# Kernel optimization log

Hardware: AMD Instinct MI355X
Metric: run time of the kernel (lower is better)

The kernel has to match this reference:

```python
import jax, jax.numpy as jnp
import numpy as np

K_HOP = 2

def _graph_conv(x, A, W, b):
    feats = [x]
    xk = x
    for _ in range(K_HOP):
        xk = jnp.einsum('bmn,bnc->bmc', A, xk)
        feats.append(xk)
    return jnp.concatenate(feats, -1) @ W + b

def _pair_mlp(y, W2, b2, W1, b1, shape):
    # normal_conv: fc1(relu(fc2(y))).reshape(shape)
    return (jax.nn.relu(y @ W2 + b2) @ W1 + b1).reshape(shape)

def setup_inputs():
    key = jax.random.key(0)
    ks = jax.random.split(key, 16)
    B, T, N = 8, 12, 200
    C_IN, H, D, H_ST = 2, 64, 32, 64
    def lin(k, fi, fo):
        k1, k2 = jax.random.split(k)
        s = 1.0 / float(np.sqrt(fi))
        return (jax.random.uniform(k1, (fi, fo), jnp.float32, -s, s),
                jax.random.uniform(k2, (fo,), jnp.float32, -s, s))
    W_s2d, b_s2d = lin(ks[0], H_ST, D)
    W_rz, b_rz = lin(ks[1], 1 + D, 2 * D)
    W_h, b_h = lin(ks[2], 1 + D, D)
    Wc2, bc2 = lin(ks[3], 2 * D, D)
    Wc1, bc1 = lin(ks[4], D, 1)
    Wm2, bm2 = lin(ks[5], 2 * D, D)
    Wm1, bm1 = lin(ks[6], D, 1)
    gin = (C_IN + H) * (1 + K_HOP)
    W_ru, b_ru = lin(ks[7], gin, 2 * H)
    W_cand, b_cand = lin(ks[8], gin, H)
    Wp1, bp1 = lin(ks[9], H, H)
    Wp2, bp2 = lin(ks[10], H, 1)
    x = jax.random.normal(ks[11], (B, T, N, C_IN), jnp.float32)
    node_fea_st = jax.random.normal(ks[12], (N, H_ST), jnp.float32)
    return dict(x=x, node_fea_st=node_fea_st, W_s2d=W_s2d, b_s2d=b_s2d,
                W_rz=W_rz, b_rz=b_rz, W_h=W_h, b_h=b_h,
                Wc2=Wc2, bc2=bc2, Wc1=Wc1, bc1=bc1,
                Wm2=Wm2, bm2=bm2, Wm1=Wm1, bm1=bm1,
                W_ru=W_ru, b_ru=b_ru, W_cand=W_cand, b_cand=b_cand,
                Wp1=Wp1, bp1=bp1, Wp2=Wp2, bp2=bp2)

def reference(x, node_fea_st, W_s2d, b_s2d, W_rz, b_rz, W_h, b_h,
              Wc2, bc2, Wc1, bc1, Wm2, bm2, Wm1, bm1,
              W_ru, b_ru, W_cand, b_cand, Wp1, bp1, Wp2, bp2):
    B, T, N, _ = x.shape
    H = W_cand.shape[1]
    D = W_h.shape[1]
    # states_dy init: linear_s2d(node_fea_st) broadcast over batch
    state_dy0 = jnp.broadcast_to((node_fea_st @ W_s2d + b_s2d)[None], (B, N, D))
    state0 = jnp.zeros((B, N, H), x.dtype)
    xs = jnp.transpose(x, (1, 0, 2, 3))  # [T,B,N,C]

    def step(carry, xt):
        state, state_dy = carry
        inp1 = xt[..., :1]
        # DynamicGraphGRU (conv_method='normal')
        rz = jax.nn.sigmoid(jnp.concatenate([inp1, state_dy], -1) @ W_rz + b_rz)
        r, z = jnp.split(rz, 2, -1)
        h = jnp.tanh(jnp.concatenate([inp1, r * state_dy], -1) @ W_h + b_h)
        new_dy = z * state_dy + (1.0 - z) * h
        s = jax.nn.relu(new_dy)  # [B,N,D]
        y = jnp.concatenate([jnp.broadcast_to(s[:, :, None, :], (B, N, N, D)),
                             jnp.broadcast_to(s[:, None, :, :], (B, N, N, D))], -1)
        g = _pair_mlp(y, Wc2, bc2, Wc1, bc1, (B, N, N))
        m = _pair_mlp(y, Wm2, bm2, Wm1, bm1, (B, N, N))
        A = g * jax.nn.sigmoid(m)  # dynamic graph [B,N,N]
        # DCGRUCell with supports=[A]
        ru = jax.nn.sigmoid(_graph_conv(jnp.concatenate([xt, state], -1), A, W_ru, b_ru))
        rr, u = jnp.split(ru, 2, -1)
        c = jnp.tanh(_graph_conv(jnp.concatenate([xt, rr * state], -1), A, W_cand, b_cand))
        new_state = u * state + (1.0 - u) * c
        return (new_state, new_dy), A

    (state, _), dy_graphs = jax.lax.scan(step, (state0, state_dy0), xs)
    # predictor: Linear -> LeakyReLU -> Linear
    pred = jax.nn.leaky_relu(state @ Wp1 + bp1) @ Wp2 + bp2  # [B,N,1]
    return pred, dy_graphs
```

## Files before the change

kernel.cpp:

```cpp
#include <hip/hip_runtime.h>
#include <math.h>

#define B_ 8
#define T_ 12
#define N_ 200
#define R_ 1600
#define NN_ 40000

__device__ __forceinline__ float sigm(float v) { return 1.f / (1.f + expf(-v)); }

__global__ void __launch_bounds__(256) k_dyall(
        const float* __restrict__ x,  const float* __restrict__ nf,
        const float* __restrict__ Ws2d, const float* __restrict__ bs2d,
        const float* __restrict__ Wrz,  const float* __restrict__ brz,
        const float* __restrict__ Wh,   const float* __restrict__ bh,
        const float* __restrict__ Wc2,  const float* __restrict__ Wm2,
        const float* __restrict__ bc2,  const float* __restrict__ bm2,
        float* __restrict__ Pc, float* __restrict__ Qc,
        float* __restrict__ Pm, float* __restrict__ Qm,
        float* __restrict__ state) {
    __shared__ float sWs2d[64 * 32], sWrz[33 * 64], sWh[33 * 32];
    __shared__ float sWc2[64 * 32], sWm2[64 * 32];
    __shared__ float sbrz[64], sbh[32], sbs2d[32], sbc2[32], sbm2[32];
    __shared__ float nfs[4][64], dy[4][32], in1[4][33], in2[4][33], rz[4][64], s4[4][32];
    int bk = blockIdx.x, tid = threadIdx.x;
    int w = tid >> 6, o = tid & 63;
    int row = bk * 4 + w, b = row / N_, n = row % N_;
    state[bk * 256 + tid] = 0.f;
    for (int idx = tid; idx < 2048; idx += 256) sWs2d[idx] = Ws2d[idx];
    for (int idx = tid; idx < 2112; idx += 256) sWrz[idx] = Wrz[idx];
    for (int idx = tid; idx < 1056; idx += 256) sWh[idx] = Wh[idx];
    for (int idx = tid; idx < 2048; idx += 256) { sWc2[idx] = Wc2[idx]; sWm2[idx] = Wm2[idx]; }
    if (tid < 64) sbrz[tid] = brz[tid];
    if (tid < 32) { sbh[tid] = bh[tid]; sbs2d[tid] = bs2d[tid];
                    sbc2[tid] = bc2[tid]; sbm2[tid] = bm2[tid]; }
    nfs[w][o] = nf[n * 64 + o];
    __syncthreads();
    if (o < 32) {
        float acc = sbs2d[o];
        #pragma unroll 8
        for (int i = 0; i < 64; ++i) acc += nfs[w][i] * sWs2d[i * 32 + o];
        dy[w][o] = acc;
    }
    __syncthreads();
    for (int t = 0; t < T_; ++t) {
        if (o == 0) { float v = x[((b * T_ + t) * N_ + n) * 2]; in1[w][0] = v; in2[w][0] = v; }
        if (o < 32) in1[w][o + 1] = dy[w][o];
        __syncthreads();
        float acc = sbrz[o];
        #pragma unroll
        for (int i = 0; i < 33; ++i) acc += in1[w][i] * sWrz[i * 64 + o];
        rz[w][o] = sigm(acc);
        __syncthreads();
        if (o < 32) in2[w][o + 1] = rz[w][o] * dy[w][o];
        __syncthreads();
        if (o < 32) {
            float h = sbh[o];
            #pragma unroll
            for (int i = 0; i < 33; ++i) h += in2[w][i] * sWh[i * 32 + o];
            h = tanhf(h);
            float z = rz[w][32 + o];
            float nd = z * dy[w][o] + (1.f - z) * h;
            dy[w][o] = nd;
            s4[w][o] = nd > 0.f ? nd : 0.f;
        }
        __syncthreads();
        size_t base = ((size_t)t * R_ + row) * 32;
        for (int idx = o; idx < 128; idx += 64) {
            int mat = idx >> 5, k = idx & 31;
            const float* W = (mat < 2) ? sWc2 : sWm2;
            int rb = (mat & 1) ? 32 : 0;
            float a = (mat == 0) ? sbc2[k] : (mat == 2) ? sbm2[k] : 0.f;
            #pragma unroll
            for (int i = 0; i < 32; ++i) a += s4[w][i] * W[(rb + i) * 32 + k];
            ((mat == 0) ? Pc : (mat == 1) ? Qc : (mat == 2) ? Pm : Qm)[base + k] = a;
        }
        __syncthreads();
    }
}

__global__ void __launch_bounds__(256) k_pairall(
        const float* __restrict__ Pc, const float* __restrict__ Qc,
        const float* __restrict__ Pm, const float* __restrict__ Qm,
        const float* __restrict__ Wc1, const float* __restrict__ bc1,
        const float* __restrict__ Wm1, const float* __restrict__ bm1,
        float* __restrict__ out) {
    __shared__ float sPc[16][36], sQc[16][36], sPm[16][36], sQm[16][36];
    __shared__ float sWc1[32], sWm1[32];
    int z = blockIdx.z;
    int i0 = blockIdx.x * 16, j0 = blockIdx.y * 16;
    int tid = threadIdx.y * 16 + threadIdx.x;
    size_t tb = (size_t)z * N_;
    for (int l = tid; l < 128; l += 256) {
        int r = l >> 3, q = l & 7;
        int gi = i0 + r, gj = j0 + r;
        float4 z4 = make_float4(0.f, 0.f, 0.f, 0.f);
        *(float4*)&sPc[r][4 * q] = (gi < N_) ? *(const float4*)&Pc[(tb + gi) * 32 + 4 * q] : z4;
        *(float4*)&sPm[r][4 * q] = (gi < N_) ? *(const float4*)&Pm[(tb + gi) * 32 + 4 * q] : z4;
        *(float4*)&sQc[r][4 * q] = (gj < N_) ? *(const float4*)&Qc[(tb + gj) * 32 + 4 * q] : z4;
        *(float4*)&sQm[r][4 * q] = (gj < N_) ? *(const float4*)&Qm[(tb + gj) * 32 + 4 * q] : z4;
    }
    if (tid < 32) { sWc1[tid] = Wc1[tid]; sWm1[tid] = Wm1[tid]; }
    __syncthreads();
    int i = i0 + threadIdx.y, j = j0 + threadIdx.x;
    if (i >= N_ || j >= N_) return;
    int ty = threadIdx.y, tx = threadIdx.x;
    float g0 = 0.f, g1 = 0.f, m0 = 0.f, m1 = 0.f;
    #pragma unroll
    for (int kg = 0; kg < 8; ++kg) {
        float4 pc = *(const float4*)&sPc[ty][4 * kg];
        float4 qc = *(const float4*)&sQc[tx][4 * kg];
        float4 wc = *(const float4*)&sWc1[4 * kg];
        g0 += fmaxf(pc.x + qc.x, 0.f) * wc.x + fmaxf(pc.y + qc.y, 0.f) * wc.y;
        g1 += fmaxf(pc.z + qc.z, 0.f) * wc.z + fmaxf(pc.w + qc.w, 0.f) * wc.w;
        float4 pm = *(const float4*)&sPm[ty][4 * kg];
        float4 qm = *(const float4*)&sQm[tx][4 * kg];
        float4 wm = *(const float4*)&sWm1[4 * kg];
        m0 += fmaxf(pm.x + qm.x, 0.f) * wm.x + fmaxf(pm.y + qm.y, 0.f) * wm.y;
        m1 += fmaxf(pm.z + qm.z, 0.f) * wm.z + fmaxf(pm.w + qm.w, 0.f) * wm.w;
    }
    float g = g0 + g1 + bc1[0];
    float m = m0 + m1 + bm1[0];
    out[R_ + (((size_t)z * N_ + i) * N_ + j)] = g * sigm(m);
}

__global__ void __launch_bounds__(256) k_a2(
        const float* __restrict__ Abase, float* __restrict__ Cbase, int nmat) {
    __shared__ float Ast[32][132];
    __shared__ float Bs[32][68];
    int bx = blockIdx.x;
    int z = bx % nmat, tl = bx / nmat;
    int i0 = (tl >> 2) * 128, j0 = (tl & 3) * 64;
    const float* Az = Abase + (size_t)z * NN_;
    float* Cz = Cbase + (size_t)z * NN_;
    int tid = threadIdx.x;
    int tx = tid & 15, ty = tid >> 4;
    float acc[8][4] = {};
    for (int k0 = 0; k0 < 200; k0 += 32) {
        {
            int i = tid >> 1;
            int kb = (tid & 1) * 16;
            int gi = i0 + i;
            #pragma unroll
            for (int q = 0; q < 4; ++q) {
                int k = kb + q * 4;
                int gk = k0 + k;
                float4 v = make_float4(0.f, 0.f, 0.f, 0.f);
                if (gi < N_) {
                    if (gk + 3 < N_) v = *(const float4*)&Az[gi * N_ + gk];
                    else {
                        float t0 = (gk + 0 < N_) ? Az[gi * N_ + gk + 0] : 0.f;
                        float t1 = (gk + 1 < N_) ? Az[gi * N_ + gk + 1] : 0.f;
                        float t2 = (gk + 2 < N_) ? Az[gi * N_ + gk + 2] : 0.f;
                        float t3 = (gk + 3 < N_) ? Az[gi * N_ + gk + 3] : 0.f;
                        v = make_float4(t0, t1, t2, t3);
                    }
                }
                Ast[k + 0][i] = v.x; Ast[k + 1][i] = v.y;
                Ast[k + 2][i] = v.z; Ast[k + 3][i] = v.w;
            }
        }
        {
            #pragma unroll
            for (int q = 0; q < 2; ++q) {
                int id = tid + 256 * q;
                int k = id >> 4, jq = (id & 15) * 4;
                int gk = k0 + k, gj = j0 + jq;
                float4 v = make_float4(0.f, 0.f, 0.f, 0.f);
                if (gk < N_) {
                    if (gj + 3 < N_) v = *(const float4*)&Az[gk * N_ + gj];
                    else {
                        float t0 = (gj + 0 < N_) ? Az[gk * N_ + gj + 0] : 0.f;
                        float t1 = (gj + 1 < N_) ? Az[gk * N_ + gj + 1] : 0.f;
                        float t2 = (gj + 2 < N_) ? Az[gk * N_ + gj + 2] : 0.f;
                        float t3 = (gj + 3 < N_) ? Az[gk * N_ + gj + 3] : 0.f;
                        v = make_float4(t0, t1, t2, t3);
                    }
                }
                *(float4*)&Bs[k][jq] = v;
            }
        }
        __syncthreads();
        #pragma unroll 8
        for (int k = 0; k < 32; ++k) {
            float4 a0 = *(const float4*)&Ast[k][ty * 8];
            float4 a1 = *(const float4*)&Ast[k][ty * 8 + 4];
            float4 bv = *(const float4*)&Bs[k][tx * 4];
            acc[0][0] += a0.x * bv.x; acc[0][1] += a0.x * bv.y; acc[0][2] += a0.x * bv.z; acc[0][3] += a0.x * bv.w;
            acc[1][0] += a0.y * bv.x; acc[1][1] += a0.y * bv.y; acc[1][2] += a0.y * bv.z; acc[1][3] += a0.y * bv.w;
            acc[2][0] += a0.z * bv.x; acc[2][1] += a0.z * bv.y; acc[2][2] += a0.z * bv.z; acc[2][3] += a0.z * bv.w;
            acc[3][0] += a0.w * bv.x; acc[3][1] += a0.w * bv.y; acc[3][2] += a0.w * bv.z; acc[3][3] += a0.w * bv.w;
            acc[4][0] += a1.x * bv.x; acc[4][1] += a1.x * bv.y; acc[4][2] += a1.x * bv.z; acc[4][3] += a1.x * bv.w;
            acc[5][0] += a1.y * bv.x; acc[5][1] += a1.y * bv.y; acc[5][2] += a1.y * bv.z; acc[5][3] += a1.y * bv.w;
            acc[6][0] += a1.z * bv.x; acc[6][1] += a1.z * bv.y; acc[6][2] += a1.z * bv.z; acc[6][3] += a1.z * bv.w;
            acc[7][0] += a1.w * bv.x; acc[7][1] += a1.w * bv.y; acc[7][2] += a1.w * bv.z; acc[7][3] += a1.w * bv.w;
        }
        __syncthreads();
    }
    #pragma unroll
    for (int r = 0; r < 8; ++r) {
        int gi = i0 + ty * 8 + r;
        if (gi >= N_) continue;
        int gj = j0 + tx * 4;
        if (gj + 3 < N_) {
            *(float4*)&Cz[gi * N_ + gj] = make_float4(acc[r][0], acc[r][1], acc[r][2], acc[r][3]);
        } else {
            #pragma unroll
            for (int e = 0; e < 4; ++e) if (gj + e < N_) Cz[gi * N_ + gj + e] = acc[r][e];
        }
    }
}

__global__ void __launch_bounds__(256) k_xh(
        const float* __restrict__ Abase, const float* __restrict__ A2base,
        const float* __restrict__ x, int z0, float* __restrict__ xh) {
    __shared__ float xtl[400];
    int zl = blockIdx.x, tid = threadIdx.x;
    int z = z0 + zl, t = z >> 3, b = z & 7;
    int w = tid >> 6, l = tid & 63;
    const float* xb = x + ((size_t)(b * T_ + t)) * N_ * 2;
    for (int idx = tid; idx < 400; idx += 256) xtl[idx] = xb[idx];
    __syncthreads();
    for (int it = 0; it < 50; ++it) {
        int i = it * 4 + w;
        float p0 = 0.f, p1 = 0.f, p2 = 0.f, p3 = 0.f;
        if (l < 50) {
            float4 a4 = *(const float4*)(Abase + (size_t)zl * NN_ + i * 200 + 4 * l);
            float4 c4 = *(const float4*)(A2base + (size_t)zl * NN_ + i * 200 + 4 * l);
            #pragma unroll
            for (int q = 0; q < 4; ++q) {
                float av = (&a4.x)[q], cv = (&c4.x)[q];
                float x0 = xtl[(4 * l + q) * 2], x1 = xtl[(4 * l + q) * 2 + 1];
                p0 += av * x0; p1 += av * x1; p2 += cv * x0; p3 += cv * x1;
            }
        }
        #pragma unroll
        for (int off = 32; off > 0; off >>= 1) {
            p0 += __shfl_down(p0, off); p1 += __shfl_down(p1, off);
            p2 += __shfl_down(p2, off); p3 += __shfl_down(p3, off);
        }
        if (l == 0) *(float4*)(xh + ((size_t)zl * N_ + i) * 4) = make_float4(p0, p1, p2, p3);
    }
}

__global__ void __launch_bounds__(256) k_ru2(
        const float* __restrict__ At, const float* __restrict__ A2t,
        const float* __restrict__ xht,
        const float* __restrict__ x, int t, const float* __restrict__ state,
        const float* __restrict__ Wru, const float* __restrict__ bru,
        float* __restrict__ rs, float* __restrict__ ub) {
    __shared__ float a2s[2 * 200], c2s[2 * 200];
    __shared__ float hpA[4][64], hpC[4][64];
    __shared__ float feat[2][200];
    __shared__ float gp[8][2][128];
    int bx = blockIdx.x;
    int b = bx & 7, i0 = (bx >> 3) * 2;
    int tid = threadIdx.x;
    const float* F = state + (size_t)b * (N_ * 64);
    {
        const float4* Ar = (const float4*)(At + ((size_t)b * N_ + i0) * 200);
        const float4* Cr = (const float4*)(A2t + ((size_t)b * N_ + i0) * 200);
        if (tid < 100) { ((float4*)a2s)[tid] = Ar[tid]; ((float4*)c2s)[tid] = Cr[tid]; }
        if (tid >= 100 && tid < 164) {
            int l = tid - 100, r = l >> 5, q = l & 31;
            *(float2*)&feat[r][2 + 2 * q] = *(const float2*)&F[(size_t)(i0 + r) * 64 + 2 * q];
        }
        if (tid >= 164 && tid < 168) {
            int l = tid - 164;
            feat[l >> 1][l & 1] = x[((size_t)(b * T_ + t) * N_ + i0 + (l >> 1)) * 2 + (l & 1)];
        }
        if (tid >= 168 && tid < 176) {
            int l = tid - 168, rr = l >> 2, q = l & 3;
            feat[rr][(q < 2) ? (66 + q) : (132 + q - 2)] = xht[((size_t)b * N_ + i0 + rr) * 4 + q];
        }
    }
    __syncthreads();
    {
        int w = tid >> 6, lane = tid & 63;
        int r = w & 1, h = w >> 1;
        int cg = lane & 15, jq = lane >> 4;
        const float* ar = a2s + r * 200 + h * 100;
        const float* cr = c2s + r * 200 + h * 100;
        const float* Fb = F + (size_t)(h * 100) * 64 + 4 * cg;
        float4 accA = make_float4(0.f, 0.f, 0.f, 0.f);
        float4 accC = make_float4(0.f, 0.f, 0.f, 0.f);
        #pragma unroll 5
        for (int m = 0; m < 25; ++m) {
            int j = jq + 4 * m;
            float av = ar[j], cv = cr[j];
            float4 f4 = *(const float4*)&Fb[(size_t)j * 64];
            accA.x += av * f4.x; accA.y += av * f4.y; accA.z += av * f4.z; accA.w += av * f4.w;
            accC.x += cv * f4.x; accC.y += cv * f4.y; accC.z += cv * f4.z; accC.w += cv * f4.w;
        }
        accA.x += __shfl_xor(accA.x, 16); accA.y += __shfl_xor(accA.y, 16);
        accA.z += __shfl_xor(accA.z, 16); accA.w += __shfl_xor(accA.w, 16);
        accC.x += __shfl_xor(accC.x, 16); accC.y += __shfl_xor(accC.y, 16);
        accC.z += __shfl_xor(accC.z, 16); accC.w += __shfl_xor(accC.w, 16);
        accA.x += __shfl_xor(accA.x, 32); accA.y += __shfl_xor(accA.y, 32);
        accA.z += __shfl_xor(accA.z, 32); accA.w += __shfl_xor(accA.w, 32);
        accC.x += __shfl_xor(accC.x, 32); accC.y += __shfl_xor(accC.y, 32);
        accC.z += __shfl_xor(accC.z, 32); accC.w += __shfl_xor(accC.w, 32);
        if (lane < 16) {
            *(float4*)&hpA[w][4 * cg] = accA;
            *(float4*)&hpC[w][4 * cg] = accC;
        }
    }
    __syncthreads();
    {
        int mt = tid >> 7, r = (tid >> 6) & 1, c = tid & 63;
        float v = mt ? (hpC[r][c] + hpC[2 + r][c]) : (hpA[r][c] + hpA[2 + r][c]);
        feat[r][(mt ? 134 : 68) + c] = v;
    }
    __syncthreads();
    {
        int cq = tid & 31, kh = tid >> 5;
        int k0 = 25 * kh, kend = (k0 + 25 < 198) ? (k0 + 25) : 198;
        float4 s0 = make_float4(0.f, 0.f, 0.f, 0.f);
        float4 s1 = make_float4(0.f, 0.f, 0.f, 0.f);
        for (int k = k0; k < kend; ++k) {
            float4 w4 = *(const float4*)&Wru[(size_t)k * 128 + 4 * cq];
            float f0 = feat[0][k], f1 = feat[1][k];
            s0.x += f0 * w4.x; s0.y += f0 * w4.y; s0.z += f0 * w4.z; s0.w += f0 * w4.w;
            s1.x += f1 * w4.x; s1.y += f1 * w4.y; s1.z += f1 * w4.z; s1.w += f1 * w4.w;
        }
        *(float4*)&gp[kh][0][4 * cq] = s0;
        *(float4*)&gp[kh][1][4 * cq] = s1;
    }
    __syncthreads();
    {
        int rq = tid >> 7, c = tid & 127;
        float a = bru[c];
        #pragma unroll
        for (int h = 0; h < 8; ++h) a += gp[h][rq][c];
        float v = sigm(a);
        size_t go = (size_t)b * N_ + i0 + rq;
        if (c < 64) rs[go * 64 + c] = v * feat[rq][2 + c];
        else        ub[go * 64 + (c - 64)] = v;
    }
}

__global__ void __launch_bounds__(256) k_cand2(
        const float* __restrict__ At, const float* __restrict__ A2t,
        const float* __restrict__ xht,
        const float* __restrict__ x, int t, const float* __restrict__ rsin,
        const float* __restrict__ Wcd, const float* __restrict__ bcd,
        const float* __restrict__ ub, float* __restrict__ state) {
    __shared__ float a2s[2 * 200], c2s[2 * 200];
    __shared__ float hpA[4][64], hpC[4][64];
    __shared__ float feat[2][200];
    __shared__ float gp[16][2][64];
    int bx = blockIdx.x;
    int b = bx & 7, i0 = (bx >> 3) * 2;
    int tid = threadIdx.x;
    const float* F = rsin + (size_t)b * (N_ * 64);
    {
        const float4* Ar = (const float4*)(At + ((size_t)b * N_ + i0) * 200);
        const float4* Cr = (const float4*)(A2t + ((size_t)b * N_ + i0) * 200);
        if (tid < 100) { ((float4*)a2s)[tid] = Ar[tid]; ((float4*)c2s)[tid] = Cr[tid]; }
        if (tid >= 100 && tid < 164) {
            int l = tid - 100, r = l >> 5, q = l & 31;
            *(float2*)&feat[r][2 + 2 * q] = *(const float2*)&F[(size_t)(i0 + r) * 64 + 2 * q];
        }
        if (tid >= 164 && tid < 168) {
            int l = tid - 164;
            feat[l >> 1][l & 1] = x[((size_t)(b * T_ + t) * N_ + i0 + (l >> 1)) * 2 + (l & 1)];
        }
        if (tid >= 168 && tid < 176) {
            int l = tid - 168, rr = l >> 2, q = l & 3;
            feat[rr][(q < 2) ? (66 + q) : (132 + q - 2)] = xht[((size_t)b * N_ + i0 + rr) * 4 + q];
        }
    }
    __syncthreads();
    {
        int w = tid >> 6, lane = tid & 63;
        int r = w & 1, h = w >> 1;
        int cg = lane & 15, jq = lane >> 4;
        const float* ar = a2s + r * 200 + h * 100;
        const float* cr = c2s + r * 200 + h * 100;
        const float* Fb = F + (size_t)(h * 100) * 64 + 4 * cg;
        float4 accA = make_float4(0.f, 0.f, 0.f, 0.f);
        float4 accC = make_float4(0.f, 0.f, 0.f, 0.f);
        #pragma unroll 5
        for (int m = 0; m < 25; ++m) {
            int j = jq + 4 * m;
            float av = ar[j], cv = cr[j];
            float4 f4 = *(const float4*)&Fb[(size_t)j * 64];
            accA.x += av * f4.x; accA.y += av * f4.y; accA.z += av * f4.z; accA.w += av * f4.w;
            accC.x += cv * f4.x; accC.y += cv * f4.y; accC.z += cv * f4.z; accC.w += cv * f4.w;
        }
        accA.x += __shfl_xor(accA.x, 16); accA.y += __shfl_xor(accA.y, 16);
        accA.z += __shfl_xor(accA.z, 16); accA.w += __shfl_xor(accA.w, 16);
        accC.x += __shfl_xor(accC.x, 16); accC.y += __shfl_xor(accC.y, 16);
        accC.z += __shfl_xor(accC.z, 16); accC.w += __shfl_xor(accC.w, 16);
        accA.x += __shfl_xor(accA.x, 32); accA.y += __shfl_xor(accA.y, 32);
        accA.z += __shfl_xor(accA.z, 32); accA.w += __shfl_xor(accA.w, 32);
        accC.x += __shfl_xor(accC.x, 32); accC.y += __shfl_xor(accC.y, 32);
        accC.z += __shfl_xor(accC.z, 32); accC.w += __shfl_xor(accC.w, 32);
        if (lane < 16) {
            *(float4*)&hpA[w][4 * cg] = accA;
            *(float4*)&hpC[w][4 * cg] = accC;
        }
    }
    __syncthreads();
    {
        int mt = tid >> 7, r = (tid >> 6) & 1, c = tid & 63;
        float v = mt ? (hpC[r][c] + hpC[2 + r][c]) : (hpA[r][c] + hpA[2 + r][c]);
        feat[r][(mt ? 134 : 68) + c] = v;
    }
    __syncthreads();
    {
        int cq = tid & 15, kh = tid >> 4;
        int k0 = 13 * kh, kend = (k0 + 13 < 198) ? (k0 + 13) : 198;
        float4 s0 = make_float4(0.f, 0.f, 0.f, 0.f);
        float4 s1 = make_float4(0.f, 0.f, 0.f, 0.f);
        for (int k = k0; k < kend; ++k) {
            float4 w4 = *(const float4*)&Wcd[(size_t)k * 64 + 4 * cq];
            float f0 = feat[0][k], f1 = feat[1][k];
            s0.x += f0 * w4.x; s0.y += f0 * w4.y; s0.z += f0 * w4.z; s0.w += f0 * w4.w;
            s1.x += f1 * w4.x; s1.y += f1 * w4.y; s1.z += f1 * w4.z; s1.w += f1 * w4.w;
        }
        *(float4*)&gp[kh][0][4 * cq] = s0;
        *(float4*)&gp[kh][1][4 * cq] = s1;
    }
    __syncthreads();
    if (tid < 128) {
        int rq = tid >> 6, c = tid & 63;
        float a = bcd[c];
        #pragma unroll
        for (int h = 0; h < 16; ++h) a += gp[h][rq][c];
        size_t go = (size_t)b * N_ + i0 + rq;
        float cnd = tanhf(a);
        float u = ub[go * 64 + c];
        float st = state[go * 64 + c];
        state[go * 64 + c] = u * st + (1.f - u) * cnd;
    }
}

__global__ void __launch_bounds__(64) k_pred(
        const float* __restrict__ state,
        const float* __restrict__ Wp1, const float* __restrict__ bp1,
        const float* __restrict__ Wp2, const float* __restrict__ bp2,
        float* __restrict__ out) {
    __shared__ float st[64];
    int row = blockIdx.x;
    int tid = threadIdx.x;
    st[tid] = state[row * 64 + tid];
    __syncthreads();
    float acc = bp1[tid];
    #pragma unroll 8
    for (int a = 0; a < 64; ++a) acc += st[a] * Wp1[a * 64 + tid];
    acc = acc > 0.f ? acc : 0.01f * acc;
    float v = acc * Wp2[tid];
    #pragma unroll
    for (int off = 32; off > 0; off >>= 1) v += __shfl_down(v, off);
    if (tid == 0) out[row] = v + bp2[0];
}

extern "C" void kernel_launch(void* const* d_in, const int* in_sizes, int n_in,
                              void* d_out, int out_size, void* d_ws, size_t ws_size,
                              hipStream_t stream) {
    const float* x    = (const float*)d_in[0];
    const float* nf   = (const float*)d_in[1];
    const float* Ws2d = (const float*)d_in[2];
    const float* bs2d = (const float*)d_in[3];
    const float* Wrz  = (const float*)d_in[4];
    const float* brz  = (const float*)d_in[5];
    const float* Wh   = (const float*)d_in[6];
    const float* bh   = (const float*)d_in[7];
    const float* Wc2  = (const float*)d_in[8];
    const float* bc2  = (const float*)d_in[9];
    const float* Wc1  = (const float*)d_in[10];
    const float* bc1  = (const float*)d_in[11];
    const float* Wm2  = (const float*)d_in[12];
    const float* bm2  = (const float*)d_in[13];
    const float* Wm1  = (const float*)d_in[14];
    const float* bm1  = (const float*)d_in[15];
    const float* Wru  = (const float*)d_in[16];
    const float* bru  = (const float*)d_in[17];
    const float* Wcand= (const float*)d_in[18];
    const float* bcand= (const float*)d_in[19];
    const float* Wp1  = (const float*)d_in[20];
    const float* bp1  = (const float*)d_in[21];
    const float* Wp2  = (const float*)d_in[22];
    const float* bp2  = (const float*)d_in[23];
    float* out = (float*)d_out;

    float* ws = (float*)d_ws;
    const size_t PQ = (size_t)T_ * R_ * 32;
    float* Pc = ws;
    float* Qc = Pc + PQ;
    float* Pm = Qc + PQ;
    float* Qm = Pm + PQ;

    const size_t A2F = (size_t)96 * NN_;
    const size_t XHF = (size_t)96 * N_ * 4;
    const size_t FULL_NEED = (A2F + XHF + 3 * (size_t)R_ * 64) * 4;
    bool full = ws_size >= FULL_NEED;

    const float* Aall = out + R_;

    if (full) {
        float* A2base = ws;
        float* xhbase = ws + A2F;
        float* state  = xhbase + XHF;
        float* rs     = state + (size_t)R_ * 64;
        float* ub     = rs + (size_t)R_ * 64;

        k_dyall<<<400, 256, 0, stream>>>(x, nf, Ws2d, bs2d, Wrz, brz, Wh, bh,
                                         Wc2, Wm2, bc2, bm2, Pc, Qc, Pm, Qm, state);
        k_pairall<<<dim3(13, 13, 96), dim3(16, 16), 0, stream>>>(
            Pc, Qc, Pm, Qm, Wc1, bc1, Wm1, bm1, out);
        k_a2<<<96 * 8, 256, 0, stream>>>(Aall, A2base, 96);
        k_xh<<<96, 256, 0, stream>>>(Aall, A2base, x, 0, xhbase);

        for (int t = 0; t < T_; ++t) {
            const float* At  = Aall + (size_t)t * 8 * NN_;
            const float* A2t = A2base + (size_t)t * 8 * NN_;
            const float* xht = xhbase + (size_t)t * 8 * N_ * 4;
            k_ru2  <<<800, 256, 0, stream>>>(At, A2t, xht, x, t, state, Wru, bru, rs, ub);
            k_cand2<<<800, 256, 0, stream>>>(At, A2t, xht, x, t, rs, Wcand, bcand, ub, state);
        }
        k_pred<<<R_, 64, 0, stream>>>(state, Wp1, bp1, Wp2, bp2, out);
    } else {
        float* A2base = ws + 4 * PQ;
        float* xhbase = A2base + (size_t)8 * NN_;
        float* state  = xhbase + (size_t)8 * N_ * 4;
        float* rs     = state + (size_t)R_ * 64;
        float* ub     = rs + (size_t)R_ * 64;

        k_dyall<<<400, 256, 0, stream>>>(x, nf, Ws2d, bs2d, Wrz, brz, Wh, bh,
                                         Wc2, Wm2, bc2, bm2, Pc, Qc, Pm, Qm, state);
        k_pairall<<<dim3(13, 13, 96), dim3(16, 16), 0, stream>>>(
            Pc, Qc, Pm, Qm, Wc1, bc1, Wm1, bm1, out);
        for (int t = 0; t < T_; ++t) {
            const float* At = Aall + (size_t)t * 8 * NN_;
            k_a2<<<8 * 8, 256, 0, stream>>>(At, A2base, 8);
            k_xh<<<8, 256, 0, stream>>>(At, A2base, x, t * 8, xhbase);
            k_ru2  <<<800, 256, 0, stream>>>(At, A2base, xhbase, x, t, state, Wru, bru, rs, ub);
            k_cand2<<<800, 256, 0, stream>>>(At, A2base, xhbase, x, t, rs, Wcand, bcand, ub, state);
        }
        k_pred<<<R_, 64, 0, stream>>>(state, Wp1, bp1, Wp2, bp2, out);
    }
}
```

Before: 477.4 us.

## Process four rows per block in DCGRU ru/cand kernels to reuse loads

The per-step ru and candidate graph-conv kernels now handle four node rows per block instead of two, halving the grid to 400 blocks. Each loaded feature float4 (and each weight float4 in the linear stage) is reused across four rows, which cuts global and L2 traffic per output. The inner diffusion loop is retiled to 8 column groups by 8 j-lanes, and shared memory use per block roughly doubles. The cost is fewer blocks per step, which may underfill the GPU's compute units, plus more registers per thread.

```diff
diff --git a/kernel.cpp b/kernel.cpp
--- a/kernel.cpp
+++ b/kernel.cpp
@@ -249,93 +249,115 @@
         const float* __restrict__ x, int t, const float* __restrict__ state,
         const float* __restrict__ Wru, const float* __restrict__ bru,
         float* __restrict__ rs, float* __restrict__ ub) {
-    __shared__ float a2s[2 * 200], c2s[2 * 200];
-    __shared__ float hpA[4][64], hpC[4][64];
-    __shared__ float feat[2][200];
-    __shared__ float gp[8][2][128];
+    __shared__ float a4s[4 * 200], c4s[4 * 200];
+    __shared__ float hpA[2][4][64], hpC[2][4][64];
+    __shared__ float feat[4][200];
+    __shared__ float gps[8][4][128];
     int bx = blockIdx.x;
-    int b = bx & 7, i0 = (bx >> 3) * 2;
+    int b = bx & 7, i0 = (bx >> 3) * 4;
     int tid = threadIdx.x;
     const float* F = state + (size_t)b * (N_ * 64);
     {
         const float4* Ar = (const float4*)(At + ((size_t)b * N_ + i0) * 200);
         const float4* Cr = (const float4*)(A2t + ((size_t)b * N_ + i0) * 200);
-        if (tid < 100) { ((float4*)a2s)[tid] = Ar[tid]; ((float4*)c2s)[tid] = Cr[tid]; }
-        if (tid >= 100 && tid < 164) {
-            int l = tid - 100, r = l >> 5, q = l & 31;
-            *(float2*)&feat[r][2 + 2 * q] = *(const float2*)&F[(size_t)(i0 + r) * 64 + 2 * q];
-        }
-        if (tid >= 164 && tid < 168) {
-            int l = tid - 164;
+        if (tid < 200) { ((float4*)a4s)[tid] = Ar[tid]; ((float4*)c4s)[tid] = Cr[tid]; }
+        { int r = tid >> 6, c = tid & 63;
+          feat[r][2 + c] = F[(size_t)(i0 + r) * 64 + c]; }
+        if (tid >= 224 && tid < 232) {
+            int l = tid - 224;
             feat[l >> 1][l & 1] = x[((size_t)(b * T_ + t) * N_ + i0 + (l >> 1)) * 2 + (l & 1)];
         }
-        if (tid >= 168 && tid < 176) {
-            int l = tid - 168, rr = l >> 2, q = l & 3;
+        if (tid >= 232 && tid < 248) {
+            int l = tid - 232, rr = l >> 2, q = l & 3;
             feat[rr][(q < 2) ? (66 + q) : (132 + q - 2)] = xht[((size_t)b * N_ + i0 + rr) * 4 + q];
         }
     }
     __syncthreads();
     {
         int w = tid >> 6, lane = tid & 63;
-        int r = w & 1, h = w >> 1;
-        int cg = lane & 15, jq = lane >> 4;
-        const float* ar = a2s + r * 200 + h * 100;
-        const float* cr = c2s + r * 200 + h * 100;
-        const float* Fb = F + (size_t)(h * 100) * 64 + 4 * cg;
-        float4 accA = make_float4(0.f, 0.f, 0.f, 0.f);
-        float4 accC = make_float4(0.f, 0.f, 0.f, 0.f);
-        #pragma unroll 5
-        for (int m = 0; m < 25; ++m) {
-            int j = jq + 4 * m;
-            float av = ar[j], cv = cr[j];
-            float4 f4 = *(const float4*)&Fb[(size_t)j * 64];
-            accA.x += av * f4.x; accA.y += av * f4.y; accA.z += av * f4.z; accA.w += av * f4.w;
-            accC.x += cv * f4.x; accC.y += cv * f4.y; accC.z += cv * f4.z; accC.w += cv * f4.w;
-        }
-        accA.x += __shfl_xor(accA.x, 16); accA.y += __shfl_xor(accA.y, 16);
-        accA.z += __shfl_xor(accA.z, 16); accA.w += __shfl_xor(accA.w, 16);
-        accC.x += __shfl_xor(accC.x, 16); accC.y += __shfl_xor(accC.y, 16);
-        accC.z += __shfl_xor(accC.z, 16); accC.w += __shfl_xor(accC.w, 16);
-        accA.x += __shfl_xor(accA.x, 32); accA.y += __shfl_xor(accA.y, 32);
-        accA.z += __shfl_xor(accA.z, 32); accA.w += __shfl_xor(accA.w, 32);
-        accC.x += __shfl_xor(accC.x, 32); accC.y += __shfl_xor(accC.y, 32);
-        accC.z += __shfl_xor(accC.z, 32); accC.w += __shfl_xor(accC.w, 32);
-        if (lane < 16) {
-            *(float4*)&hpA[w][4 * cg] = accA;
-            *(float4*)&hpC[w][4 * cg] = accC;
-        }
-    }
-    __syncthreads();
-    {
-        int mt = tid >> 7, r = (tid >> 6) & 1, c = tid & 63;
-        float v = mt ? (hpC[r][c] + hpC[2 + r][c]) : (hpA[r][c] + hpA[2 + r][c]);
-        feat[r][(mt ? 134 : 68) + c] = v;
+        int h = w >> 1, ch = w & 1;
+        int cg = lane & 7, jq = lane >> 3;
+        int colb = ch * 32 + 4 * cg;
+        const float* Fb = F + (size_t)(h * 100) * 64 + colb;
+        const float* ab = a4s + h * 100;
+        const float* cb = c4s + h * 100;
+        float4 accA[4], accC[4];
+        #pragma unroll
+        for (int r = 0; r < 4; ++r) {
+            accA[r] = make_float4(0.f, 0.f, 0.f, 0.f);
+            accC[r] = make_float4(0.f, 0.f, 0.f, 0.f);
+        }
+        #pragma unroll 4
+        for (int m = 0; m < 13; ++m) {
+            int jo = jq + 8 * m;
+            if (jo < 100) {
+                float4 f4 = *(const float4*)&Fb[(size_t)jo * 64];
+                #pragma unroll
+                for (int r = 0; r < 4; ++r) {
+                    float av = ab[r * 200 + jo], cv = cb[r * 200 + jo];
+                    accA[r].x += av * f4.x; accA[r].y += av * f4.y;
+                    accA[r].z += av * f4.z; accA[r].w += av * f4.w;
+                    accC[r].x += cv * f4.x; accC[r].y += cv * f4.y;
+                    accC[r].z += cv * f4.z; accC[r].w += cv * f4.w;
+                }
+            }
+        }
+        #pragma unroll
+        for (int off = 8; off <= 32; off <<= 1) {
+            #pragma unroll
+            for (int r = 0; r < 4; ++r) {
+                accA[r].x += __shfl_xor(accA[r].x, off); accA[r].y += __shfl_xor(accA[r].y, off);
+                accA[r].z += __shfl_xor(accA[r].z, off); accA[r].w += __shfl_xor(accA[r].w, off);
+                accC[r].x += __shfl_xor(accC[r].x, off); accC[r].y += __shfl_xor(accC[r].y, off);
+                accC[r].z += __shfl_xor(accC[r].z, off); accC[r].w += __shfl_xor(accC[r].w, off);
+            }
+        }
+        if (lane < 8) {
+            #pragma unroll
+            for (int r = 0; r < 4; ++r) {
+                *(float4*)&hpA[h][r][colb] = accA[r];
+                *(float4*)&hpC[h][r][colb] = accC[r];
+            }
+        }
+    }
+    __syncthreads();
+    {
+        int r = tid >> 6, c = tid & 63;
+        feat[r][68 + c]  = hpA[0][r][c] + hpA[1][r][c];
+        feat[r][134 + c] = hpC[0][r][c] + hpC[1][r][c];
     }
     __syncthreads();
     {
         int cq = tid & 31, kh = tid >> 5;
         int k0 = 25 * kh, kend = (k0 + 25 < 198) ? (k0 + 25) : 198;
-        float4 s0 = make_float4(0.f, 0.f, 0.f, 0.f);
-        float4 s1 = make_float4(0.f, 0.f, 0.f, 0.f);
+        float4 s0 = make_float4(0.f, 0.f, 0.f, 0.f), s1 = s0, s2 = s0, s3 = s0;
         for (int k = k0; k < kend; ++k) {
             float4 w4 = *(const float4*)&Wru[(size_t)k * 128 + 4 * cq];
-            float f0 = feat[0][k], f1 = feat[1][k];
+            float f0 = feat[0][k], f1 = feat[1][k], f2 = feat[2][k], f3 = feat[3][k];
             s0.x += f0 * w4.x; s0.y += f0 * w4.y; s0.z += f0 * w4.z; s0.w += f0 * w4.w;
             s1.x += f1 * w4.x; s1.y += f1 * w4.y; s1.z += f1 * w4.z; s1.w += f1 * w4.w;
-        }
-        *(float4*)&gp[kh][0][4 * cq] = s0;
-        *(float4*)&gp[kh][1][4 * cq] = s1;
+            s2.x += f2 * w4.x; s2.y += f2 * w4.y; s2.z += f2 * w4.z; s2.w += f2 * w4.w;
+            s3.x += f3 * w4.x; s3.y += f3 * w4.y; s3.z += f3 * w4.z; s3.w += f3 * w4.w;
+        }
+        *(float4*)&gps[kh][0][4 * cq] = s0;
+        *(float4*)&gps[kh][1][4 * cq] = s1;
+        *(float4*)&gps[kh][2][4 * cq] = s2;
+        *(float4*)&gps[kh][3][4 * cq] = s3;
     }
     __syncthreads();
     {
         int rq = tid >> 7, c = tid & 127;
-        float a = bru[c];
-        #pragma unroll
-        for (int h = 0; h < 8; ++h) a += gp[h][rq][c];
-        float v = sigm(a);
-        size_t go = (size_t)b * N_ + i0 + rq;
-        if (c < 64) rs[go * 64 + c] = v * feat[rq][2 + c];
-        else        ub[go * 64 + (c - 64)] = v;
+        #pragma unroll
+        for (int rr = 0; rr < 2; ++rr) {
+            int r = rq * 2 + rr;
+            float a = bru[c];
+            #pragma unroll
+            for (int h = 0; h < 8; ++h) a += gps[h][r][c];
+            float v = sigm(a);
+            size_t go = (size_t)b * N_ + i0 + r;
+            if (c < 64) rs[go * 64 + c] = v * feat[r][2 + c];
+            else        ub[go * 64 + (c - 64)] = v;
+        }
     }
 }
 
@@ -345,90 +367,108 @@
         const float* __restrict__ x, int t, const float* __restrict__ rsin,
         const float* __restrict__ Wcd, const float* __restrict__ bcd,
         const float* __restrict__ ub, float* __restrict__ state) {
-    __shared__ float a2s[2 * 200], c2s[2 * 200];
-    __shared__ float hpA[4][64], hpC[4][64];
-    __shared__ float feat[2][200];
-    __shared__ float gp[16][2][64];
+    __shared__ float a4s[4 * 200], c4s[4 * 200];
+    __shared__ float hpA[2][4][64], hpC[2][4][64];
+    __shared__ float feat[4][200];
+    __shared__ float gps[16][4][64];
     int bx = blockIdx.x;
-    int b = bx & 7, i0 = (bx >> 3) * 2;
+    int b = bx & 7, i0 = (bx >> 3) * 4;
     int tid = threadIdx.x;
     const float* F = rsin + (size_t)b * (N_ * 64);
     {
         const float4* Ar = (const float4*)(At + ((size_t)b * N_ + i0) * 200);
         const float4* Cr = (const float4*)(A2t + ((size_t)b * N_ + i0) * 200);
-        if (tid < 100) { ((float4*)a2s)[tid] = Ar[tid]; ((float4*)c2s)[tid] = Cr[tid]; }
-        if (tid >= 100 && tid < 164) {
-            int l = tid - 100, r = l >> 5, q = l & 31;
-            *(float2*)&feat[r][2 + 2 * q] = *(const float2*)&F[(size_t)(i0 + r) * 64 + 2 * q];
-        }
-        if (tid >= 164 && tid < 168) {
-            int l = tid - 164;
+        if (tid < 200) { ((float4*)a4s)[tid] = Ar[tid]; ((float4*)c4s)[tid] = Cr[tid]; }
+        { int r = tid >> 6, c = tid & 63;
+          feat[r][2 + c] = F[(size_t)(i0 + r) * 64 + c]; }
+        if (tid >= 224 && tid < 232) {
+            int l = tid - 224;
             feat[l >> 1][l & 1] = x[((size_t)(b * T_ + t) * N_ + i0 + (l >> 1)) * 2 + (l & 1)];
         }
-        if (tid >= 168 && tid < 176) {
-            int l = tid - 168, rr = l >> 2, q = l & 3;
+        if (tid >= 232 && tid < 248) {
+            int l = tid - 232, rr = l >> 2, q = l & 3;
             feat[rr][(q < 2) ? (66 + q) : (132 + q - 2)] = xht[((size_t)b * N_ + i0 + rr) * 4 + q];
         }
     }
     __syncthreads();
     {
         int w = tid >> 6, lane = tid & 63;
-        int r = w & 1, h = w >> 1;
-        int cg = lane & 15, jq = lane >> 4;
-        const float* ar = a2s + r * 200 + h * 100;
-        const float* cr = c2s + r * 200 + h * 100;
-        const float* Fb = F + (size_t)(h * 100) * 64 + 4 * cg;
-        float4 accA = make_float4(0.f, 0.f, 0.f, 0.f);
-        float4 accC = make_float4(0.f, 0.f, 0.f, 0.f);
-        #pragma unroll 5
-        for (int m = 0; m < 25; ++m) {
-            int j = jq + 4 * m;
-            float av = ar[j], cv = cr[j];
-            float4 f4 = *(const float4*)&Fb[(size_t)j * 64];
-            accA.x += av * f4.x; accA.y += av * f4.y; accA.z += av * f4.z; accA.w += av * f4.w;
-            accC.x += cv * f4.x; accC.y += cv * f4.y; accC.z += cv * f4.z; accC.w += cv * f4.w;
-        }
-        accA.x += __shfl_xor(accA.x, 16); accA.y += __shfl_xor(accA.y, 16);
-        accA.z += __shfl_xor(accA.z, 16); accA.w += __shfl_xor(accA.w, 16);
-        accC.x += __shfl_xor(accC.x, 16); accC.y += __shfl_xor(accC.y, 16);
-        accC.z += __shfl_xor(accC.z, 16); accC.w += __shfl_xor(accC.w, 16);
-        accA.x += __shfl_xor(accA.x, 32); accA.y += __shfl_xor(accA.y, 32);
-        accA.z += __shfl_xor(accA.z, 32); accA.w += __shfl_xor(accA.w, 32);
-        accC.x += __shfl_xor(accC.x, 32); accC.y += __shfl_xor(accC.y, 32);
-        accC.z += __shfl_xor(accC.z, 32); accC.w += __shfl_xor(accC.w, 32);
-        if (lane < 16) {
-            *(float4*)&hpA[w][4 * cg] = accA;
-            *(float4*)&hpC[w][4 * cg] = accC;
-        }
-    }
-    __syncthreads();
-    {
-        int mt = tid >> 7, r = (tid >> 6) & 1, c = tid & 63;
-        float v = mt ? (hpC[r][c] + hpC[2 + r][c]) : (hpA[r][c] + hpA[2 + r][c]);
-        feat[r][(mt ? 134 : 68) + c] = v;
+        int h = w >> 1, ch = w & 1;
+        int cg = lane & 7, jq = lane >> 3;
+        int colb = ch * 32 + 4 * cg;
+        const float* Fb = F + (size_t)(h * 100) * 64 + colb;
+        const float* ab = a4s + h * 100;
+        const float* cb = c4s + h * 100;
+        float4 accA[4], accC[4];
+        #pragma unroll
+        for (int r = 0; r < 4; ++r) {
+            accA[r] = make_float4(0.f, 0.f, 0.f, 0.f);
+            accC[r] = make_float4(0.f, 0.f, 0.f, 0.f);
+        }
+        #pragma unroll 4
+        for (int m = 0; m < 13; ++m) {
+            int jo = jq + 8 * m;
+            if (jo < 100) {
+                float4 f4 = *(const float4*)&Fb[(size_t)jo * 64];
+                #pragma unroll
+                for (int r = 0; r < 4; ++r) {
+                    float av = ab[r * 200 + jo], cv = cb[r * 200 + jo];
+                    accA[r].x += av * f4.x; accA[r].y += av * f4.y;
+                    accA[r].z += av * f4.z; accA[r].w += av * f4.w;
+                    accC[r].x += cv * f4.x; accC[r].y += cv * f4.y;
+                    accC[r].z += cv * f4.z; accC[r].w += cv * f4.w;
+                }
+            }
+        }
+        #pragma unroll
+        for (int off = 8; off <= 32; off <<= 1) {
+            #pragma unroll
+            for (int r = 0; r < 4; ++r) {
+                accA[r].x += __shfl_xor(accA[r].x, off); accA[r].y += __shfl_xor(accA[r].y, off);
+                accA[r].z += __shfl_xor(accA[r].z, off); accA[r].w += __shfl_xor(accA[r].w, off);
+                accC[r].x += __shfl_xor(accC[r].x, off); accC[r].y += __shfl_xor(accC[r].y, off);
+                accC[r].z += __shfl_xor(accC[r].z, off); accC[r].w += __shfl_xor(accC[r].w, off);
+            }
+        }
+        if (lane < 8) {
+            #pragma unroll
+            for (int r = 0; r < 4; ++r) {
+                *(float4*)&hpA[h][r][colb] = accA[r];
+                *(float4*)&hpC[h][r][colb] = accC[r];
+            }
+        }
+    }
+    __syncthreads();
+    {
+        int r = tid >> 6, c = tid & 63;
+        feat[r][68 + c]  = hpA[0][r][c] + hpA[1][r][c];
+        feat[r][134 + c] = hpC[0][r][c] + hpC[1][r][c];
     }
     __syncthreads();
     {
         int cq = tid & 15, kh = tid >> 4;
         int k0 = 13 * kh, kend = (k0 + 13 < 198) ? (k0 + 13) : 198;
-        float4 s0 = make_float4(0.f, 0.f, 0.f, 0.f);
-        float4 s1 = make_float4(0.f, 0.f, 0.f, 0.f);
+        float4 s0 = make_float4(0.f, 0.f, 0.f, 0.f), s1 = s0, s2 = s0, s3 = s0;
         for (int k = k0; k < kend; ++k) {
             float4 w4 = *(const float4*)&Wcd[(size_t)k * 64 + 4 * cq];
-            float f0 = feat[0][k], f1 = feat[1][k];
+            float f0 = feat[0][k], f1 = feat[1][k], f2 = feat[2][k], f3 = feat[3][k];
             s0.x += f0 * w4.x; s0.y += f0 * w4.y; s0.z += f0 * w4.z; s0.w += f0 * w4.w;
             s1.x += f1 * w4.x; s1.y += f1 * w4.y; s1.z += f1 * w4.z; s1.w += f1 * w4.w;
-        }
-        *(float4*)&gp[kh][0][4 * cq] = s0;
-        *(float4*)&gp[kh][1][4 * cq] = s1;
-    }
-    __syncthreads();
-    if (tid < 128) {
-        int rq = tid >> 6, c = tid & 63;
+            s2.x += f2 * w4.x; s2.y += f2 * w4.y; s2.z += f2 * w4.z; s2.w += f2 * w4.w;
+            s3.x += f3 * w4.x; s3.y += f3 * w4.y; s3.z += f3 * w4.z; s3.w += f3 * w4.w;
+        }
+        *(float4*)&gps[kh][0][4 * cq] = s0;
+        *(float4*)&gps[kh][1][4 * cq] = s1;
+        *(float4*)&gps[kh][2][4 * cq] = s2;
+        *(float4*)&gps[kh][3][4 * cq] = s3;
+    }
+    __syncthreads();
+    {
+        int r = tid >> 6, c = tid & 63;
         float a = bcd[c];
         #pragma unroll
-        for (int h = 0; h < 16; ++h) a += gp[h][rq][c];
-        size_t go = (size_t)b * N_ + i0 + rq;
+        for (int h = 0; h < 16; ++h) a += gps[h][r][c];
+        size_t go = (size_t)b * N_ + i0 + r;
         float cnd = tanhf(a);
         float u = ub[go * 64 + c];
         float st = state[go * 64 + c];
@@ -517,8 +557,8 @@
             const float* At  = Aall + (size_t)t * 8 * NN_;
             const float* A2t = A2base + (size_t)t * 8 * NN_;
             const float* xht = xhbase + (size_t)t * 8 * N_ * 4;
-            k_ru2  <<<800, 256, 0, stream>>>(At, A2t, xht, x, t, state, Wru, bru, rs, ub);
-            k_cand2<<<800, 256, 0, stream>>>(At, A2t, xht, x, t, rs, Wcand, bcand, ub, state);
+            k_ru2  <<<400, 256, 0, stream>>>(At, A2t, xht, x, t, state, Wru, bru, rs, ub);
+            k_cand2<<<400, 256, 0, stream>>>(At, A2t, xht, x, t, rs, Wcand, bcand, ub, state);
         }
         k_pred<<<R_, 64, 0, stream>>>(state, Wp1, bp1, Wp2, bp2, out);
     } else {
@@ -536,8 +576,8 @@
             const float* At = Aall + (size_t)t * 8 * NN_;
             k_a2<<<8 * 8, 256, 0, stream>>>(At, A2base, 8);
             k_xh<<<8, 256, 0, stream>>>(At, A2base, x, t * 8, xhbase);
-            k_ru2  <<<800, 256, 0, stream>>>(At, A2base, xhbase, x, t, state, Wru, bru, rs, ub);
-            k_cand2<<<800, 256, 0, stream>>>(At, A2base, xhbase, x, t, rs, Wcand, bcand, ub, state);
+            k_ru2  <<<400, 256, 0, stream>>>(At, A2base, xhbase, x, t, state, Wru, bru, rs, ub);
+            k_cand2<<<400, 256, 0, stream>>>(At, A2base, xhbase, x, t, rs, Wcand, bcand, ub, state);
         }
         k_pred<<<R_, 64, 0, stream>>>(state, Wp1, bp1, Wp2, bp2, out);
     }
```

Measured after the change: 516.6 us. +8.2%, slower.

## Register-block pair MLP to 2x2 outputs per thread and transpose dy weights

Applied to the files above, without the earlier changes.

The pair kernel now computes a 32x32 tile per block with each thread producing four outputs, so each P/Q vector loaded from shared memory is reused twice. The final-layer weights now live in registers instead of shared memory. In the dynamic-state kernel, the weight matrices are stored transposed and padded so the dot products can use float4 shared-memory reads. The cost is higher register pressure and fewer blocks in the pair kernel.

```diff
diff --git a/kernel.cpp b/kernel.cpp
--- a/kernel.cpp
+++ b/kernel.cpp
@@ -19,18 +19,34 @@
         float* __restrict__ Pc, float* __restrict__ Qc,
         float* __restrict__ Pm, float* __restrict__ Qm,
         float* __restrict__ state) {
-    __shared__ float sWs2d[64 * 32], sWrz[33 * 64], sWh[33 * 32];
-    __shared__ float sWc2[64 * 32], sWm2[64 * 32];
+    __shared__ alignas(16) float sWs2d[64 * 32];
+    __shared__ alignas(16) float sWrzT[64][36];
+    __shared__ alignas(16) float sWhT[32][36];
+    __shared__ alignas(16) float sWc2T[32][68];
+    __shared__ alignas(16) float sWm2T[32][68];
     __shared__ float sbrz[64], sbh[32], sbs2d[32], sbc2[32], sbm2[32];
-    __shared__ float nfs[4][64], dy[4][32], in1[4][33], in2[4][33], rz[4][64], s4[4][32];
+    __shared__ alignas(16) float nfs[4][64], dy[4][32], rz[4][64], s4[4][32];
+    __shared__ alignas(16) float in1[4][36], in2[4][36];
     int bk = blockIdx.x, tid = threadIdx.x;
     int w = tid >> 6, o = tid & 63;
     int row = bk * 4 + w, b = row / N_, n = row % N_;
     state[bk * 256 + tid] = 0.f;
     for (int idx = tid; idx < 2048; idx += 256) sWs2d[idx] = Ws2d[idx];
-    for (int idx = tid; idx < 2112; idx += 256) sWrz[idx] = Wrz[idx];
-    for (int idx = tid; idx < 1056; idx += 256) sWh[idx] = Wh[idx];
-    for (int idx = tid; idx < 2048; idx += 256) { sWc2[idx] = Wc2[idx]; sWm2[idx] = Wm2[idx]; }
+    for (int idx = tid; idx < 2304; idx += 256) {
+        int oo = idx / 36, ii = idx % 36;
+        sWrzT[oo][ii] = (ii < 33) ? Wrz[ii * 64 + oo] : 0.f;
+    }
+    for (int idx = tid; idx < 1152; idx += 256) {
+        int kk = idx / 36, ii = idx % 36;
+        sWhT[kk][ii] = (ii < 33) ? Wh[ii * 32 + kk] : 0.f;
+    }
+    for (int idx = tid; idx < 2176; idx += 256) {
+        int kk = idx / 68, rr = idx % 68;
+        float vc = (rr < 64) ? Wc2[rr * 32 + kk] : 0.f;
+        float vm = (rr < 64) ? Wm2[rr * 32 + kk] : 0.f;
+        sWc2T[kk][rr] = vc; sWm2T[kk][rr] = vm;
+    }
+    if (tid < 144) { ((float*)in1)[tid] = 0.f; ((float*)in2)[tid] = 0.f; }
     if (tid < 64) sbrz[tid] = brz[tid];
     if (tid < 32) { sbh[tid] = bh[tid]; sbs2d[tid] = bs2d[tid];
                     sbc2[tid] = bc2[tid]; sbm2[tid] = bm2[tid]; }
@@ -49,7 +65,11 @@
         __syncthreads();
         float acc = sbrz[o];
         #pragma unroll
-        for (int i = 0; i < 33; ++i) acc += in1[w][i] * sWrz[i * 64 + o];
+        for (int ig = 0; ig < 9; ++ig) {
+            float4 w4 = *(const float4*)&sWrzT[o][4 * ig];
+            float4 f4 = *(const float4*)&in1[w][4 * ig];
+            acc += f4.x * w4.x + f4.y * w4.y + f4.z * w4.z + f4.w * w4.w;
+        }
         rz[w][o] = sigm(acc);
         __syncthreads();
         if (o < 32) in2[w][o + 1] = rz[w][o] * dy[w][o];
@@ -57,7 +77,11 @@
         if (o < 32) {
             float h = sbh[o];
             #pragma unroll
-            for (int i = 0; i < 33; ++i) h += in2[w][i] * sWh[i * 32 + o];
+            for (int ig = 0; ig < 9; ++ig) {
+                float4 w4 = *(const float4*)&sWhT[o][4 * ig];
+                float4 f4 = *(const float4*)&in2[w][4 * ig];
+                h += f4.x * w4.x + f4.y * w4.y + f4.z * w4.z + f4.w * w4.w;
+            }
             h = tanhf(h);
             float z = rz[w][32 + o];
             float nd = z * dy[w][o] + (1.f - z) * h;
@@ -68,11 +92,15 @@
         size_t base = ((size_t)t * R_ + row) * 32;
         for (int idx = o; idx < 128; idx += 64) {
             int mat = idx >> 5, k = idx & 31;
-            const float* W = (mat < 2) ? sWc2 : sWm2;
+            const float* WT = (mat < 2) ? &sWc2T[k][0] : &sWm2T[k][0];
             int rb = (mat & 1) ? 32 : 0;
             float a = (mat == 0) ? sbc2[k] : (mat == 2) ? sbm2[k] : 0.f;
             #pragma unroll
-            for (int i = 0; i < 32; ++i) a += s4[w][i] * W[(rb + i) * 32 + k];
+            for (int ig = 0; ig < 8; ++ig) {
+                float4 w4 = *(const float4*)&WT[rb + 4 * ig];
+                float4 f4 = *(const float4*)&s4[w][4 * ig];
+                a += f4.x * w4.x + f4.y * w4.y + f4.z * w4.z + f4.w * w4.w;
+            }
             ((mat == 0) ? Pc : (mat == 1) ? Qc : (mat == 2) ? Pm : Qm)[base + k] = a;
         }
         __syncthreads();
@@ -85,43 +113,70 @@
         const float* __restrict__ Wc1, const float* __restrict__ bc1,
         const float* __restrict__ Wm1, const float* __restrict__ bm1,
         float* __restrict__ out) {
-    __shared__ float sPc[16][36], sQc[16][36], sPm[16][36], sQm[16][36];
-    __shared__ float sWc1[32], sWm1[32];
+    __shared__ alignas(16) float sPc[32][36], sPm[32][36], sQc[32][36], sQm[32][36];
     int z = blockIdx.z;
-    int i0 = blockIdx.x * 16, j0 = blockIdx.y * 16;
+    int i0 = blockIdx.x * 32, j0 = blockIdx.y * 32;
     int tid = threadIdx.y * 16 + threadIdx.x;
     size_t tb = (size_t)z * N_;
-    for (int l = tid; l < 128; l += 256) {
-        int r = l >> 3, q = l & 7;
+    float4 z4 = make_float4(0.f, 0.f, 0.f, 0.f);
+    {
+        int r = tid >> 3, q = tid & 7;
         int gi = i0 + r, gj = j0 + r;
-        float4 z4 = make_float4(0.f, 0.f, 0.f, 0.f);
         *(float4*)&sPc[r][4 * q] = (gi < N_) ? *(const float4*)&Pc[(tb + gi) * 32 + 4 * q] : z4;
         *(float4*)&sPm[r][4 * q] = (gi < N_) ? *(const float4*)&Pm[(tb + gi) * 32 + 4 * q] : z4;
         *(float4*)&sQc[r][4 * q] = (gj < N_) ? *(const float4*)&Qc[(tb + gj) * 32 + 4 * q] : z4;
         *(float4*)&sQm[r][4 * q] = (gj < N_) ? *(const float4*)&Qm[(tb + gj) * 32 + 4 * q] : z4;
     }
-    if (tid < 32) { sWc1[tid] = Wc1[tid]; sWm1[tid] = Wm1[tid]; }
-    __syncthreads();
-    int i = i0 + threadIdx.y, j = j0 + threadIdx.x;
-    if (i >= N_ || j >= N_) return;
-    int ty = threadIdx.y, tx = threadIdx.x;
-    float g0 = 0.f, g1 = 0.f, m0 = 0.f, m1 = 0.f;
+    float4 wc[8], wm[8];
     #pragma unroll
     for (int kg = 0; kg < 8; ++kg) {
-        float4 pc = *(const float4*)&sPc[ty][4 * kg];
-        float4 qc = *(const float4*)&sQc[tx][4 * kg];
-        float4 wc = *(const float4*)&sWc1[4 * kg];
-        g0 += fmaxf(pc.x + qc.x, 0.f) * wc.x + fmaxf(pc.y + qc.y, 0.f) * wc.y;
-        g1 += fmaxf(pc.z + qc.z, 0.f) * wc.z + fmaxf(pc.w + qc.w, 0.f) * wc.w;
-        float4 pm = *(const float4*)&sPm[ty][4 * kg];
-        float4 qm = *(const float4*)&sQm[tx][4 * kg];
-        float4 wm = *(const float4*)&sWm1[4 * kg];
-        m0 += fmaxf(pm.x + qm.x, 0.f) * wm.x + fmaxf(pm.y + qm.y, 0.f) * wm.y;
-        m1 += fmaxf(pm.z + qm.z, 0.f) * wm.z + fmaxf(pm.w + qm.w, 0.f) * wm.w;
-    }
-    float g = g0 + g1 + bc1[0];
-    float m = m0 + m1 + bm1[0];
-    out[R_ + (((size_t)z * N_ + i) * N_ + j)] = g * sigm(m);
+        wc[kg] = *(const float4*)&Wc1[4 * kg];
+        wm[kg] = *(const float4*)&Wm1[4 * kg];
+    }
+    __syncthreads();
+    int ty = threadIdx.y, tx = threadIdx.x;
+    float gAA = 0.f, gAB = 0.f, gBA = 0.f, gBB = 0.f;
+    float mAA = 0.f, mAB = 0.f, mBA = 0.f, mBB = 0.f;
+    #pragma unroll
+    for (int kg = 0; kg < 8; ++kg) {
+        float4 pA = *(const float4*)&sPc[ty][4 * kg];
+        float4 pB = *(const float4*)&sPc[16 + ty][4 * kg];
+        float4 qA = *(const float4*)&sQc[tx][4 * kg];
+        float4 qB = *(const float4*)&sQc[16 + tx][4 * kg];
+        float4 w4 = wc[kg];
+        gAA += fmaxf(pA.x + qA.x, 0.f) * w4.x + fmaxf(pA.y + qA.y, 0.f) * w4.y
+             + fmaxf(pA.z + qA.z, 0.f) * w4.z + fmaxf(pA.w + qA.w, 0.f) * w4.w;
+        gAB += fmaxf(pA.x + qB.x, 0.f) * w4.x + fmaxf(pA.y + qB.y, 0.f) * w4.y
+             + fmaxf(pA.z + qB.z, 0.f) * w4.z + fmaxf(pA.w + qB.w, 0.f) * w4.w;
+        gBA += fmaxf(pB.x + qA.x, 0.f) * w4.x + fmaxf(pB.y + qA.y, 0.f) * w4.y
+             + fmaxf(pB.z + qA.z, 0.f) * w4.z + fmaxf(pB.w + qA.w, 0.f) * w4.w;
+        gBB += fmaxf(pB.x + qB.x, 0.f) * w4.x + fmaxf(pB.y + qB.y, 0.f) * w4.y
+             + fmaxf(pB.z + qB.z, 0.f) * w4.z + fmaxf(pB.w + qB.w, 0.f) * w4.w;
+        float4 nA = *(const float4*)&sPm[ty][4 * kg];
+        float4 nB = *(const float4*)&sPm[16 + ty][4 * kg];
+        float4 rA = *(const float4*)&sQm[tx][4 * kg];
+        float4 rB = *(const float4*)&sQm[16 + tx][4 * kg];
+        float4 v4 = wm[kg];
+        mAA += fmaxf(nA.x + rA.x, 0.f) * v4.x + fmaxf(nA.y + rA.y, 0.f) * v4.y
+             + fmaxf(nA.z + rA.z, 0.f) * v4.z + fmaxf(nA.w + rA.w, 0.f) * v4.w;
+        mAB += fmaxf(nA.x + rB.x, 0.f) * v4.x + fmaxf(nA.y + rB.y, 0.f) * v4.y
+             + fmaxf(nA.z + rB.z, 0.f) * v4.z + fmaxf(nA.w + rB.w, 0.f) * v4.w;
+        mBA += fmaxf(nB.x + rA.x, 0.f) * v4.x + fmaxf(nB.y + rA.y, 0.f) * v4.y
+             + fmaxf(nB.z + rA.z, 0.f) * v4.z + fmaxf(nB.w + rA.w, 0.f) * v4.w;
+        mBB += fmaxf(nB.x + rB.x, 0.f) * v4.x + fmaxf(nB.y + rB.y, 0.f) * v4.y
+             + fmaxf(nB.z + rB.z, 0.f) * v4.z + fmaxf(nB.w + rB.w, 0.f) * v4.w;
+    }
+    float bg = bc1[0], bm = bm1[0];
+    int iA = i0 + ty, iB = iA + 16, jA = j0 + tx, jB = jA + 16;
+    size_t zb = R_ + (size_t)z * N_ * N_;
+    if (iA < N_) {
+        if (jA < N_) out[zb + (size_t)iA * N_ + jA] = (gAA + bg) * sigm(mAA + bm);
+        if (jB < N_) out[zb + (size_t)iA * N_ + jB] = (gAB + bg) * sigm(mAB + bm);
+    }
+    if (iB < N_) {
+        if (jA < N_) out[zb + (size_t)iB * N_ + jA] = (gBA + bg) * sigm(mBA + bm);
+        if (jB < N_) out[zb + (size_t)iB * N_ + jB] = (gBB + bg) * sigm(mBB + bm);
+    }
 }
 
 __global__ void __launch_bounds__(256) k_a2(
@@ -508,7 +563,7 @@
 
         k_dyall<<<400, 256, 0, stream>>>(x, nf, Ws2d, bs2d, Wrz, brz, Wh, bh,
                                          Wc2, Wm2, bc2, bm2, Pc, Qc, Pm, Qm, state);
-        k_pairall<<<dim3(13, 13, 96), dim3(16, 16), 0, stream>>>(
+        k_pairall<<<dim3(7, 7, 96), dim3(16, 16), 0, stream>>>(
             Pc, Qc, Pm, Qm, Wc1, bc1, Wm1, bm1, out);
         k_a2<<<96 * 8, 256, 0, stream>>>(Aall, A2base, 96);
         k_xh<<<96, 256, 0, stream>>>(Aall, A2base, x, 0, xhbase);
@@ -530,7 +585,7 @@
 
         k_dyall<<<400, 256, 0, stream>>>(x, nf, Ws2d, bs2d, Wrz, brz, Wh, bh,
                                          Wc2, Wm2, bc2, bm2, Pc, Qc, Pm, Qm, state);
-        k_pairall<<<dim3(13, 13, 96), dim3(16, 16), 0, stream>>>(
+        k_pairall<<<dim3(7, 7, 96), dim3(16, 16), 0, stream>>>(
             Pc, Qc, Pm, Qm, Wc1, bc1, Wm1, bm1, out);
         for (int t = 0; t < T_; ++t) {
             const float* At = Aall + (size_t)t * 8 * NN_;
```

Result: slower. 505.4 us (+5.8%).
